# Optimization experiments

Hardware: AMD Instinct MI355X
Metric: run time of the kernel (lower is better)

Reference implementation:

```python
import jax, jax.numpy as jnp
import numpy as np

N_NODES = 100000
N_EDGES = 600000
N_GRAPHS = 128
IN_DIM = 4
HID = 32
HEADS1 = 4
NEG_SLOPE = 0.2


def _segment_softmax(e, seg, n):
    # e: [E, H], softmax over edges sharing the same destination node
    m = jax.ops.segment_max(e, seg, num_segments=n)
    ex = jnp.exp(e - m[seg])
    s = jax.ops.segment_sum(ex, seg, num_segments=n)
    return ex / s[seg]


def _gat_layer(x, src, dst, W, a_src, a_dst, b, heads, ch):
    # PyG GATConv: h = x W (per-head), alpha = softmax_dst(leaky_relu(a_s.h_src + a_d.h_dst))
    n = x.shape[0]
    h = (x @ W).reshape(n, heads, ch)                       # [N, H, C]
    al_s = jnp.einsum('nhc,hc->nh', h, a_src)               # [N, H]
    al_d = jnp.einsum('nhc,hc->nh', h, a_dst)
    e = jax.nn.leaky_relu(al_s[src] + al_d[dst], NEG_SLOPE)  # [E, H]
    alpha = _segment_softmax(e, dst, n)                      # [E, H]
    msg = h[src] * alpha[:, :, None]                         # [E, H, C]
    out = jax.ops.segment_sum(msg, dst, num_segments=n)     # [N, H, C]
    return out.reshape(n, heads * ch) + b


def setup_inputs() -> dict:
    key = jax.random.key(0)
    ks = jax.random.split(key, 16)
    s = 0.1
    return {
        'x': jax.random.normal(ks[0], (N_NODES, IN_DIM), jnp.float32),
        'edge_index': jax.random.randint(ks[1], (2, N_EDGES), 0, N_NODES, jnp.int64),
        'batch': jax.random.randint(ks[2], (N_NODES,), 0, N_GRAPHS, jnp.int64),
        'W1': jax.random.normal(ks[3], (IN_DIM, HEADS1 * HID), jnp.float32) * s,
        'a_s1': jax.random.normal(ks[4], (HEADS1, HID), jnp.float32) * s,
        'a_d1': jax.random.normal(ks[5], (HEADS1, HID), jnp.float32) * s,
        'b1': jnp.zeros((HEADS1 * HID,), jnp.float32),
        'W2': jax.random.normal(ks[6], (HEADS1 * HID, HID), jnp.float32) * s,
        'a_s2': jax.random.normal(ks[7], (1, HID), jnp.float32) * s,
        'a_d2': jax.random.normal(ks[8], (1, HID), jnp.float32) * s,
        'b2': jnp.zeros((HID,), jnp.float32),
        'Wc1': jax.random.normal(ks[9], (HID, 32), jnp.float32) * s,
        'bc1': jnp.zeros((32,), jnp.float32),
        'Wc2': jax.random.normal(ks[10], (32, 1), jnp.float32) * s,
        'bc2': jnp.zeros((1,), jnp.float32),
    }


def reference(x, edge_index, batch, W1, a_s1, a_d1, b1, W2, a_s2, a_d2, b2, Wc1, bc1, Wc2, bc2):
    n = x.shape[0]
    loops = jnp.arange(n, dtype=edge_index.dtype)
    src = jnp.concatenate([edge_index[0], loops])   # add_self_loops=True (PyG default)
    dst = jnp.concatenate([edge_index[1], loops])
    h = jax.nn.elu(_gat_layer(x, src, dst, W1, a_s1, a_d1, b1, HEADS1, HID))
    h = jax.nn.elu(_gat_layer(h, src, dst, W2, a_s2, a_d2, b2, 1, HID))
    # global_mean_pool
    sums = jax.ops.segment_sum(h, batch, num_segments=N_GRAPHS)
    cnt = jax.ops.segment_sum(jnp.ones((n, 1), h.dtype), batch, num_segments=N_GRAPHS)
    g = sums / jnp.maximum(cnt, 1.0)
    z = jax.nn.relu(g @ Wc1 + bc1)
    return jax.nn.sigmoid(z @ Wc2 + bc2)
```

## Files before the change

### kernel.cpp

```cpp
#include <hip/hip_runtime.h>
#include <hip/hip_fp16.h>
#include <float.h>

#define NEG 0.2f
#define NPART 16
#define PAD 32

typedef _Float16 half8 __attribute__((ext_vector_type(8)));
typedef float f32x4 __attribute__((ext_vector_type(4)));

__device__ __forceinline__ float lrelu(float x){ return x > 0.f ? x : NEG * x; }
__device__ __forceinline__ float elu1(float x){ return x > 0.f ? x : (__expf(x) - 1.f); }

__global__ void k_scat(const int* __restrict__ ei, const int* __restrict__ batch,
                       int* __restrict__ cur, int* __restrict__ csr_src,
                       float* __restrict__ gcnt, int N, int E){
  __shared__ float gc[128];
  int tid = threadIdx.x;
  bool doh = blockIdx.x < 256;
  if (doh && tid < 128) gc[tid] = 0.f;
  __syncthreads();
  int idx = blockIdx.x * 256 + tid;
  int gstr = gridDim.x * 256;
  for (int e = idx; e < E; e += gstr){
    int s = ei[e], d = ei[E + e];
    int pos = atomicAdd(cur + d, 1);
    if (pos < PAD) csr_src[(size_t)d * PAD + pos] = s;
  }
  if (doh){
    for (int n = idx; n < N; n += 256 * 256)
      atomicAdd(&gc[batch[n]], 1.f);
    __syncthreads();
    if (tid < 128 && gc[tid] != 0.f) atomicAdd(gcnt + tid, gc[tid]);
  }
}

__global__ void __launch_bounds__(256, 6)
k_layer1(const int* __restrict__ degp, const int* __restrict__ csr_src,
         const float* __restrict__ x, const float* __restrict__ W1,
         const float* __restrict__ as1, const float* __restrict__ ad1,
         const float* __restrict__ b1, const float* __restrict__ W2,
         const float* __restrict__ as2, const float* __restrict__ ad2,
         __half* __restrict__ h2h, float* __restrict__ als2,
         float* __restrict__ ald2, int N){
  __shared__ float PQ[2][16];
  __shared__ __align__(16) float xa[32][20];
  __shared__ __align__(16) _Float16 out1sh[32][136];
  __shared__ __align__(16) float h2sh[32][36];
  __shared__ float als_s[32], ald_s[32];
  int tid = threadIdx.x;
  const float4* x4 = (const float4*)x;

  int g1 = tid >> 3, l = tid & 7;
  int node1 = blockIdx.x * 32 + g1;
  int nd = node1 < N ? node1 : N - 1;
  int deg = degp[nd];
  size_t r0 = (size_t)nd * PAD;
  int s_pre = csr_src[r0 + l];
  int total = (node1 < N) ? deg + 1 : 0;
  int s0 = (l < deg) ? s_pre : nd;
  float4 xv0 = x4[s0];
  float4 xn = x4[nd];

  if (tid < 32){
    int which = tid >> 4, kh = tid & 15, k = kh >> 2, h = kh & 3;
    const float* a = which ? ad1 : as1;
    float s = 0.f;
    #pragma unroll 8
    for (int c = 0; c < 32; c++) s += W1[k*128 + h*32 + c] * a[h*32 + c];
    PQ[which][kh] = s;
  }
  __syncthreads();

  {
    float P[16], Q[16];
    #pragma unroll
    for (int i = 0; i < 16; i++){ P[i] = PQ[0][i]; Q[i] = PQ[1][i]; }
    float ald0 = xn.x*Q[0] + xn.y*Q[4] + xn.z*Q[8]  + xn.w*Q[12];
    float ald1_ = xn.x*Q[1] + xn.y*Q[5] + xn.z*Q[9]  + xn.w*Q[13];
    float ald2_ = xn.x*Q[2] + xn.y*Q[6] + xn.z*Q[10] + xn.w*Q[14];
    float ald3 = xn.x*Q[3] + xn.y*Q[7] + xn.z*Q[11] + xn.w*Q[15];
    float acc[16];
    #pragma unroll
    for (int i = 0; i < 16; i++) acc[i] = 0.f;
    float ss[4] = {0.f, 0.f, 0.f, 0.f};
    if (l < total){
      float4 xv = xv0;
      float a0 = xv.x*P[0] + xv.y*P[4] + xv.z*P[8]  + xv.w*P[12];
      float a1 = xv.x*P[1] + xv.y*P[5] + xv.z*P[9]  + xv.w*P[13];
      float a2 = xv.x*P[2] + xv.y*P[6] + xv.z*P[10] + xv.w*P[14];
      float a3 = xv.x*P[3] + xv.y*P[7] + xv.z*P[11] + xv.w*P[15];
      float e0 = __expf(lrelu(a0 + ald0));
      float e1 = __expf(lrelu(a1 + ald1_));
      float e2 = __expf(lrelu(a2 + ald2_));
      float e3 = __expf(lrelu(a3 + ald3));
      ss[0] += e0; ss[1] += e1; ss[2] += e2; ss[3] += e3;
      acc[0]  += e0*xv.x; acc[1]  += e0*xv.y; acc[2]  += e0*xv.z; acc[3]  += e0*xv.w;
      acc[4]  += e1*xv.x; acc[5]  += e1*xv.y; acc[6]  += e1*xv.z; acc[7]  += e1*xv.w;
      acc[8]  += e2*xv.x; acc[9]  += e2*xv.y; acc[10] += e2*xv.z; acc[11] += e2*xv.w;
      acc[12] += e3*xv.x; acc[13] += e3*xv.y; acc[14] += e3*xv.z; acc[15] += e3*xv.w;
    }
    for (int t = l + 8; t < total; t += 8){
      int s = (t < deg) ? csr_src[r0 + t] : nd;
      float4 xv = x4[s];
      float a0 = xv.x*P[0] + xv.y*P[4] + xv.z*P[8]  + xv.w*P[12];
      float a1 = xv.x*P[1] + xv.y*P[5] + xv.z*P[9]  + xv.w*P[13];
      float a2 = xv.x*P[2] + xv.y*P[6] + xv.z*P[10] + xv.w*P[14];
      float a3 = xv.x*P[3] + xv.y*P[7] + xv.z*P[11] + xv.w*P[15];
      float e0 = __expf(lrelu(a0 + ald0));
      float e1 = __expf(lrelu(a1 + ald1_));
      float e2 = __expf(lrelu(a2 + ald2_));
      float e3 = __expf(lrelu(a3 + ald3));
      ss[0] += e0; ss[1] += e1; ss[2] += e2; ss[3] += e3;
      acc[0]  += e0*xv.x; acc[1]  += e0*xv.y; acc[2]  += e0*xv.z; acc[3]  += e0*xv.w;
      acc[4]  += e1*xv.x; acc[5]  += e1*xv.y; acc[6]  += e1*xv.z; acc[7]  += e1*xv.w;
      acc[8]  += e2*xv.x; acc[9]  += e2*xv.y; acc[10] += e2*xv.z; acc[11] += e2*xv.w;
      acc[12] += e3*xv.x; acc[13] += e3*xv.y; acc[14] += e3*xv.z; acc[15] += e3*xv.w;
    }
    #pragma unroll
    for (int m = 4; m >= 1; m >>= 1){
      #pragma unroll
      for (int i = 0; i < 16; i++) acc[i] += __shfl_xor(acc[i], m, 8);
      #pragma unroll
      for (int i = 0; i < 4; i++)  ss[i]  += __shfl_xor(ss[i], m, 8);
    }
    if (l == 0){
      float* o = xa[g1];
      *(float4*)(o)      = make_float4(acc[0],  acc[1],  acc[2],  acc[3]);
      *(float4*)(o + 4)  = make_float4(acc[4],  acc[5],  acc[6],  acc[7]);
      *(float4*)(o + 8)  = make_float4(acc[8],  acc[9],  acc[10], acc[11]);
      *(float4*)(o + 12) = make_float4(acc[12], acc[13], acc[14], acc[15]);
      *(float4*)(o + 16) = make_float4(ss[0], ss[1], ss[2], ss[3]);
    }
  }
  __syncthreads();
  if (tid < 128) xa[tid >> 2][16 + (tid & 3)] = 1.f / xa[tid >> 2][16 + (tid & 3)];
  __builtin_amdgcn_sched_barrier(0);

  int wv = tid >> 6, lane = tid & 63;
  int wm = wv >> 1, wn = wv & 1;
  int lrow = lane & 15, lk8 = lane >> 4;
  half8 bf[4];
  #pragma unroll
  for (int t = 0; t < 4; t++){
    #pragma unroll
    for (int j = 0; j < 8; j++)
      bf[t][j] = (_Float16)W2[(t*32 + lk8*8 + j)*32 + wn*16 + lrow];
  }
  int c128 = ((wv & 1) << 6) | lane;
  int gbase = (wv >> 1) << 4;
  int hh = c128 >> 5;
  float w1c0 = W1[c128], w1c1 = W1[128 + c128];
  float w1c2 = W1[256 + c128], w1c3 = W1[384 + c128];
  float b1c = b1[c128];
  __syncthreads();

  #pragma unroll
  for (int i = 0; i < 16; i++){
    int g = gbase + i;
    const float* xg = xa[g];
    float4 xv = *(const float4*)(xg + hh*4);
    float rs = xg[16 + hh];
    float o = elu1((xv.x*w1c0 + xv.y*w1c1 + xv.z*w1c2 + xv.w*w1c3) * rs + b1c);
    out1sh[g][c128] = (_Float16)o;
  }
  __syncthreads();

  {
    f32x4 acc2 = {0.f, 0.f, 0.f, 0.f};
    #pragma unroll
    for (int t = 0; t < 4; t++){
      half8 af = *(const half8*)(&out1sh[wm*16 + lrow][t*32 + lk8*8]);
      acc2 = __builtin_amdgcn_mfma_f32_16x16x32_f16(af, bf[t], acc2, 0, 0, 0);
    }
    #pragma unroll
    for (int i = 0; i < 4; i++)
      h2sh[wm*16 + lk8*4 + i][wn*16 + lrow] = acc2[i];
  }
  __syncthreads();

  {
    int g = tid >> 3, q = tid & 7;
    int node = blockIdx.x * 32 + g;
    float4 hv = *(const float4*)(&h2sh[g][q*4]);
    if (node < N){
      __half2 pa = __floats2half2_rn(hv.x, hv.y);
      __half2 pb = __floats2half2_rn(hv.z, hv.w);
      __half2* dst = (__half2*)(h2h + (size_t)node*32 + q*4);
      dst[0] = pa; dst[1] = pb;
    }
    float4 sa = *(const float4*)(as2 + q*4);
    float4 da = *(const float4*)(ad2 + q*4);
    float ps = hv.x*sa.x + hv.y*sa.y + hv.z*sa.z + hv.w*sa.w;
    float pd = hv.x*da.x + hv.y*da.y + hv.z*da.z + hv.w*da.w;
    #pragma unroll
    for (int m = 4; m >= 1; m >>= 1){
      ps += __shfl_xor(ps, m, 8);
      pd += __shfl_xor(pd, m, 8);
    }
    if (q == 0){ als_s[g] = ps; ald_s[g] = pd; }
  }
  __syncthreads();
  if (tid < 32){
    int node = blockIdx.x * 32 + tid;
    if (node < N){ als2[node] = als_s[tid]; ald2[node] = ald_s[tid]; }
  }
}

__global__ void __launch_bounds__(256)
k_gat2(const int* __restrict__ degp, const int* __restrict__ csr_src,
       const __half* __restrict__ h2h, const float* __restrict__ als2,
       const float* __restrict__ ald2, const float* __restrict__ b2,
       const int* __restrict__ batch, float* __restrict__ gsum_part, int N){
  int tid = threadIdx.x;
  int node = blockIdx.x * 16 + (tid >> 4);
  if (node >= N) return;
  int l = tid & 15;
  int sub = l >> 3;
  int c4 = l & 7;
  int deg = degp[node];
  size_t r0 = (size_t)node * PAD;
  int total = deg + 1;
  float ald = ald2[node];

  float ssum = 0.f;
  float f0 = 0.f, f1 = 0.f, f2 = 0.f, f3 = 0.f;
  for (int base = 0; base < total; base += 16){
    int t = base + l;
    int s = (t < deg) ? csr_src[r0 + t] : node;
    float ex = (t < total) ? __expf(lrelu(als2[s] + ald)) : 0.f;
    ssum += ex;
    int lim = min(16, total - base);
    for (int jj = 0; jj < lim; jj += 8){
      int ja = jj + sub, jb = jj + 2 + sub, jc = jj + 4 + sub, jd = jj + 6 + sub;
      float ea = __shfl(ex, ja, 16); int sa = __shfl(s, ja, 16);
      float eb = __shfl(ex, jb, 16); int sb = __shfl(s, jb, 16);
      float ec = __shfl(ex, jc, 16); int sc = __shfl(s, jc, 16);
      float ed = __shfl(ex, jd, 16); int sd = __shfl(s, jd, 16);
      union { float2 f; __half2 h[2]; } ua, ub, uc, ud;
      ua.f = *(const float2*)(h2h + (size_t)sa*32 + (c4 << 2));
      ub.f = *(const float2*)(h2h + (size_t)sb*32 + (c4 << 2));
      uc.f = *(const float2*)(h2h + (size_t)sc*32 + (c4 << 2));
      ud.f = *(const float2*)(h2h + (size_t)sd*32 + (c4 << 2));
      float2 va0 = __half22float2(ua.h[0]), va1 = __half22float2(ua.h[1]);
      float2 vb0 = __half22float2(ub.h[0]), vb1 = __half22float2(ub.h[1]);
      float2 vc0 = __half22float2(uc.h[0]), vc1 = __half22float2(uc.h[1]);
      float2 vd0 = __half22float2(ud.h[0]), vd1 = __half22float2(ud.h[1]);
      f0 += ea*va0.x + eb*vb0.x + ec*vc0.x + ed*vd0.x;
      f1 += ea*va0.y + eb*vb0.y + ec*vc0.y + ed*vd0.y;
      f2 += ea*va1.x + eb*vb1.x + ec*vc1.x + ed*vd1.x;
      f3 += ea*va1.y + eb*vb1.y + ec*vc1.y + ed*vd1.y;
    }
  }
  f0 += __shfl_xor(f0, 8, 16);
  f1 += __shfl_xor(f1, 8, 16);
  f2 += __shfl_xor(f2, 8, 16);
  f3 += __shfl_xor(f3, 8, 16);
  #pragma unroll
  for (int m = 8; m >= 1; m >>= 1) ssum += __shfl_xor(ssum, m, 16);
  float rs = 1.f / ssum;
  float va = sub ? f2 : f0;
  float vb = sub ? f3 : f1;
  int ch = (c4 << 2) + (sub << 1);
  float2 b2v = *(const float2*)(b2 + ch);
  int b = batch[node];
  float* gp = gsum_part + ((blockIdx.x & (NPART-1)) << 12) + b*32 + ch;
  atomicAdd(gp + 0, elu1(va*rs + b2v.x));
  atomicAdd(gp + 1, elu1(vb*rs + b2v.y));
}

__global__ void k_head(const float* __restrict__ gsum_part, const float* __restrict__ gcnt,
                       const float* __restrict__ Wc1, const float* __restrict__ bc1,
                       const float* __restrict__ Wc2, const float* __restrict__ bc2,
                       float* __restrict__ out){
  int g = blockIdx.x, tid = threadIdx.x;
  __shared__ float gl[32];
  if (tid < 32){
    float s = 0.f;
    #pragma unroll
    for (int p = 0; p < NPART; p++) s += gsum_part[(p << 12) + g*32 + tid];
    float cnt = gcnt[g];
    cnt = cnt > 1.f ? cnt : 1.f;
    gl[tid] = s / cnt;
  }
  __syncthreads();
  if (tid < 32){
    float z = bc1[tid];
    #pragma unroll 8
    for (int c2 = 0; c2 < 32; c2++) z += gl[c2] * Wc1[c2*32 + tid];
    z = z > 0.f ? z : 0.f;
    float r = z * Wc2[tid];
    #pragma unroll
    for (int m = 16; m >= 1; m >>= 1) r += __shfl_xor(r, m, 32);
    if (tid == 0) out[g] = 1.f / (1.f + expf(-(r + bc2[0])));
  }
}

extern "C" void kernel_launch(void* const* d_in, const int* in_sizes, int n_in,
                              void* d_out, int out_size, void* d_ws, size_t ws_size,
                              hipStream_t stream){
  const float* x   = (const float*)d_in[0];
  const int*   ei  = (const int*)d_in[1];
  const int*   bat = (const int*)d_in[2];
  const float* W1  = (const float*)d_in[3];
  const float* as1 = (const float*)d_in[4];
  const float* ad1 = (const float*)d_in[5];
  const float* b1  = (const float*)d_in[6];
  const float* W2  = (const float*)d_in[7];
  const float* as2 = (const float*)d_in[8];
  const float* ad2 = (const float*)d_in[9];
  const float* b2  = (const float*)d_in[10];
  const float* Wc1 = (const float*)d_in[11];
  const float* bc1 = (const float*)d_in[12];
  const float* Wc2 = (const float*)d_in[13];
  const float* bc2 = (const float*)d_in[14];
  float* out = (float*)d_out;

  const int N = in_sizes[2];
  const int E = in_sizes[1] / 2;

  float* ws = (float*)d_ws;
  size_t off = 0;
  int* cur    = (int*)ws;           off += (size_t)N;
  float* gsum_part = ws + off;      off += (size_t)NPART * 4096;
  float* gcnt = ws + off;           off += 128;
  const size_t zero_elems = off;
  __half* h2h = (__half*)(ws + off); off += (size_t)N * 16;
  float* als2 = ws + off;           off += (size_t)N;
  float* ald2 = ws + off;           off += (size_t)N;
  int* csr_src= (int*)(ws + off);   off += (size_t)N * PAD;

  hipMemsetAsync(d_ws, 0, zero_elems * sizeof(float), stream);

  k_scat<<<(E + 255) / 256, 256, 0, stream>>>(ei, bat, cur, csr_src, gcnt, N, E);

  k_layer1<<<(N + 31) / 32, 256, 0, stream>>>(cur, csr_src, x, W1, as1, ad1, b1,
                                              W2, as2, ad2, h2h, als2, ald2, N);

  k_gat2<<<(N + 15) / 16, 256, 0, stream>>>(cur, csr_src, h2h, als2, ald2, b2,
                                            bat, gsum_part, N);

  k_head<<<128, 64, 0, stream>>>(gsum_part, gcnt, Wc1, bc1, Wc2, bc2, out);
}
```

Baseline: 176.7 us.

## Accumulate graph pooling in shared memory with persistent gat2 blocks

```diff
diff --git a/kernel.cpp b/kernel.cpp
--- a/kernel.cpp
+++ b/kernel.cpp
@@ -3,7 +3,7 @@
 #include <float.h>
 
 #define NEG 0.2f
-#define NPART 16
+#define GPART 256
 #define PAD 32
 
 typedef _Float16 half8 __attribute__((ext_vector_type(8)));
@@ -207,81 +207,96 @@
   }
 }
 
-__global__ void __launch_bounds__(256)
+__global__ void __launch_bounds__(1024)
 k_gat2(const int* __restrict__ degp, const int* __restrict__ csr_src,
        const __half* __restrict__ h2h, const float* __restrict__ als2,
        const float* __restrict__ ald2, const float* __restrict__ b2,
        const int* __restrict__ batch, float* __restrict__ gsum_part, int N){
+  __shared__ __align__(16) float acc[128][32];
   int tid = threadIdx.x;
-  int node = blockIdx.x * 16 + (tid >> 4);
-  if (node >= N) return;
+  ((float4*)&acc[0][0])[tid] = make_float4(0.f, 0.f, 0.f, 0.f);
+  __syncthreads();
+
   int l = tid & 15;
   int sub = l >> 3;
   int c4 = l & 7;
-  int deg = degp[node];
-  size_t r0 = (size_t)node * PAD;
-  int total = deg + 1;
-  float ald = ald2[node];
-
-  float ssum = 0.f;
-  float f0 = 0.f, f1 = 0.f, f2 = 0.f, f3 = 0.f;
-  for (int base = 0; base < total; base += 16){
-    int t = base + l;
-    int s = (t < deg) ? csr_src[r0 + t] : node;
-    float ex = (t < total) ? __expf(lrelu(als2[s] + ald)) : 0.f;
-    ssum += ex;
-    int lim = min(16, total - base);
-    for (int jj = 0; jj < lim; jj += 8){
-      int ja = jj + sub, jb = jj + 2 + sub, jc = jj + 4 + sub, jd = jj + 6 + sub;
-      float ea = __shfl(ex, ja, 16); int sa = __shfl(s, ja, 16);
-      float eb = __shfl(ex, jb, 16); int sb = __shfl(s, jb, 16);
-      float ec = __shfl(ex, jc, 16); int sc = __shfl(s, jc, 16);
-      float ed = __shfl(ex, jd, 16); int sd = __shfl(s, jd, 16);
-      union { float2 f; __half2 h[2]; } ua, ub, uc, ud;
-      ua.f = *(const float2*)(h2h + (size_t)sa*32 + (c4 << 2));
-      ub.f = *(const float2*)(h2h + (size_t)sb*32 + (c4 << 2));
-      uc.f = *(const float2*)(h2h + (size_t)sc*32 + (c4 << 2));
-      ud.f = *(const float2*)(h2h + (size_t)sd*32 + (c4 << 2));
-      float2 va0 = __half22float2(ua.h[0]), va1 = __half22float2(ua.h[1]);
-      float2 vb0 = __half22float2(ub.h[0]), vb1 = __half22float2(ub.h[1]);
-      float2 vc0 = __half22float2(uc.h[0]), vc1 = __half22float2(uc.h[1]);
-      float2 vd0 = __half22float2(ud.h[0]), vd1 = __half22float2(ud.h[1]);
-      f0 += ea*va0.x + eb*vb0.x + ec*vc0.x + ed*vd0.x;
-      f1 += ea*va0.y + eb*vb0.y + ec*vc0.y + ed*vd0.y;
-      f2 += ea*va1.x + eb*vb1.x + ec*vc1.x + ed*vd1.x;
-      f3 += ea*va1.y + eb*vb1.y + ec*vc1.y + ed*vd1.y;
-    }
-  }
-  f0 += __shfl_xor(f0, 8, 16);
-  f1 += __shfl_xor(f1, 8, 16);
-  f2 += __shfl_xor(f2, 8, 16);
-  f3 += __shfl_xor(f3, 8, 16);
-  #pragma unroll
-  for (int m = 8; m >= 1; m >>= 1) ssum += __shfl_xor(ssum, m, 16);
-  float rs = 1.f / ssum;
-  float va = sub ? f2 : f0;
-  float vb = sub ? f3 : f1;
   int ch = (c4 << 2) + (sub << 1);
   float2 b2v = *(const float2*)(b2 + ch);
-  int b = batch[node];
-  float* gp = gsum_part + ((blockIdx.x & (NPART-1)) << 12) + b*32 + ch;
-  atomicAdd(gp + 0, elu1(va*rs + b2v.x));
-  atomicAdd(gp + 1, elu1(vb*rs + b2v.y));
-}
-
-__global__ void k_head(const float* __restrict__ gsum_part, const float* __restrict__ gcnt,
-                       const float* __restrict__ Wc1, const float* __restrict__ bc1,
-                       const float* __restrict__ Wc2, const float* __restrict__ bc2,
-                       float* __restrict__ out){
+
+  for (int node = blockIdx.x * 64 + (tid >> 4); node < N; node += GPART * 64){
+    int deg = degp[node];
+    size_t r0 = (size_t)node * PAD;
+    int total = deg + 1;
+    float ald = ald2[node];
+
+    float ssum = 0.f;
+    float f0 = 0.f, f1 = 0.f, f2 = 0.f, f3 = 0.f;
+    for (int base = 0; base < total; base += 16){
+      int t = base + l;
+      int s = (t < deg) ? csr_src[r0 + t] : node;
+      float ex = (t < total) ? __expf(lrelu(als2[s] + ald)) : 0.f;
+      ssum += ex;
+      int lim = min(16, total - base);
+      for (int jj = 0; jj < lim; jj += 8){
+        int ja = jj + sub, jb = jj + 2 + sub, jc = jj + 4 + sub, jd = jj + 6 + sub;
+        float ea = __shfl(ex, ja, 16); int sa = __shfl(s, ja, 16);
+        float eb = __shfl(ex, jb, 16); int sb = __shfl(s, jb, 16);
+        float ec = __shfl(ex, jc, 16); int sc = __shfl(s, jc, 16);
+        float ed = __shfl(ex, jd, 16); int sd = __shfl(s, jd, 16);
+        union { float2 f; __half2 h[2]; } ua, ub, uc, ud;
+        ua.f = *(const float2*)(h2h + (size_t)sa*32 + (c4 << 2));
+        ub.f = *(const float2*)(h2h + (size_t)sb*32 + (c4 << 2));
+        uc.f = *(const float2*)(h2h + (size_t)sc*32 + (c4 << 2));
+        ud.f = *(const float2*)(h2h + (size_t)sd*32 + (c4 << 2));
+        float2 va0 = __half22float2(ua.h[0]), va1 = __half22float2(ua.h[1]);
+        float2 vb0 = __half22float2(ub.h[0]), vb1 = __half22float2(ub.h[1]);
+        float2 vc0 = __half22float2(uc.h[0]), vc1 = __half22float2(uc.h[1]);
+        float2 vd0 = __half22float2(ud.h[0]), vd1 = __half22float2(ud.h[1]);
+        f0 += ea*va0.x + eb*vb0.x + ec*vc0.x + ed*vd0.x;
+        f1 += ea*va0.y + eb*vb0.y + ec*vc0.y + ed*vd0.y;
+        f2 += ea*va1.x + eb*vb1.x + ec*vc1.x + ed*vd1.x;
+        f3 += ea*va1.y + eb*vb1.y + ec*vc1.y + ed*vd1.y;
+      }
+    }
+    f0 += __shfl_xor(f0, 8, 16);
+    f1 += __shfl_xor(f1, 8, 16);
+    f2 += __shfl_xor(f2, 8, 16);
+    f3 += __shfl_xor(f3, 8, 16);
+    #pragma unroll
+    for (int m = 8; m >= 1; m >>= 1) ssum += __shfl_xor(ssum, m, 16);
+    float rs = 1.f / ssum;
+    float va = sub ? f2 : f0;
+    float vb = sub ? f3 : f1;
+    int b = batch[node];
+    atomicAdd(&acc[b][ch],     elu1(va*rs + b2v.x));
+    atomicAdd(&acc[b][ch + 1], elu1(vb*rs + b2v.y));
+  }
+  __syncthreads();
+  float4 v = ((const float4*)&acc[0][0])[tid];
+  *(float4*)(gsum_part + ((size_t)blockIdx.x << 12) + (tid << 2)) = v;
+}
+
+__global__ void __launch_bounds__(256)
+k_head(const float* __restrict__ gsum_part, const float* __restrict__ gcnt,
+       const float* __restrict__ Wc1, const float* __restrict__ bc1,
+       const float* __restrict__ Wc2, const float* __restrict__ bc2,
+       float* __restrict__ out){
   int g = blockIdx.x, tid = threadIdx.x;
+  __shared__ float part[8][32];
   __shared__ float gl[32];
+  int w = tid >> 5, ln = tid & 31;
+  float s = 0.f;
+  for (int p = w; p < GPART; p += 8)
+    s += gsum_part[((size_t)p << 12) + g*32 + ln];
+  part[w][ln] = s;
+  __syncthreads();
   if (tid < 32){
-    float s = 0.f;
-    #pragma unroll
-    for (int p = 0; p < NPART; p++) s += gsum_part[(p << 12) + g*32 + tid];
+    float s2 = 0.f;
+    #pragma unroll
+    for (int q = 0; q < 8; q++) s2 += part[q][tid];
     float cnt = gcnt[g];
     cnt = cnt > 1.f ? cnt : 1.f;
-    gl[tid] = s / cnt;
+    gl[tid] = s2 / cnt;
   }
   __syncthreads();
   if (tid < 32){
@@ -322,9 +337,9 @@
   float* ws = (float*)d_ws;
   size_t off = 0;
   int* cur    = (int*)ws;           off += (size_t)N;
-  float* gsum_part = ws + off;      off += (size_t)NPART * 4096;
   float* gcnt = ws + off;           off += 128;
   const size_t zero_elems = off;
+  float* gsum_part = ws + off;      off += (size_t)GPART * 4096;
   __half* h2h = (__half*)(ws + off); off += (size_t)N * 16;
   float* als2 = ws + off;           off += (size_t)N;
   float* ald2 = ws + off;           off += (size_t)N;
@@ -337,8 +352,8 @@
   k_layer1<<<(N + 31) / 32, 256, 0, stream>>>(cur, csr_src, x, W1, as1, ad1, b1,
                                               W2, as2, ad2, h2h, als2, ald2, N);
 
-  k_gat2<<<(N + 15) / 16, 256, 0, stream>>>(cur, csr_src, h2h, als2, ald2, b2,
-                                            bat, gsum_part, N);
-
-  k_head<<<128, 64, 0, stream>>>(gsum_part, gcnt, Wc1, bc1, Wc2, bc2, out);
-}
+  k_gat2<<<GPART, 1024, 0, stream>>>(cur, csr_src, h2h, als2, ald2, b2,
+                                     bat, gsum_part, N);
+
+  k_head<<<128, 256, 0, stream>>>(gsum_part, gcnt, Wc1, bc1, Wc2, bc2, out);
+}
```

Result: slower. 185.5 us (+5.0%).
